# Kernel tuning notes

Measured on AMD Instinct MI355X. Metric: run time of the kernel, lower is better.

The kernel has to match this reference:

```python
import jax, jax.numpy as jnp
import numpy as np

U = 50000
I = 25000
D = 128
NUM_INTERACTIONS = 800000
NUM_LAYERS = 3


def setup_inputs() -> dict:
    key = jax.random.key(0)
    k1, k2, k3, k4 = jax.random.split(key, 4)
    # LightGCN init: nn.init.normal_(emb.weight, std=1e-4)
    user_emb = jax.random.normal(k1, (U, D), dtype=jnp.float32) * 1e-4
    item_emb = jax.random.normal(k2, (I, D), dtype=jnp.float32) * 1e-4
    # Bipartite interactions; item node ids offset by U. Symmetric adjacency.
    u = jax.random.randint(k3, (NUM_INTERACTIONS,), 0, U, dtype=jnp.int32)
    it = jax.random.randint(k4, (NUM_INTERACTIONS,), U, U + I, dtype=jnp.int32)
    edge_src = jnp.concatenate([u, it])  # [E] destination rows of adj_t
    edge_dst = jnp.concatenate([it, u])  # [E] source cols (neighbors)
    return {"user_emb": user_emb, "item_emb": item_emb,
            "edge_src": edge_src, "edge_dst": edge_dst}


def reference(user_emb, item_emb, edge_src, edge_dst):
    N = U + I
    x = jnp.concatenate([user_emb, item_emb], axis=0)  # [N, D]
    # gcn_norm without self-loops: w_ij = deg_i^-1/2 * deg_j^-1/2
    ones = jnp.ones(edge_src.shape[0], dtype=x.dtype)
    deg = jax.ops.segment_sum(ones, edge_src, num_segments=N)
    dinv = jnp.where(deg > 0, jax.lax.rsqrt(jnp.maximum(deg, 1.0)), 0.0)
    w = dinv[edge_src] * dinv[edge_dst]  # [E]
    scale = 1.0 / (NUM_LAYERS + 1)
    avg = x * scale
    for _ in range(NUM_LAYERS):
        # SpMM: out[i] = sum_{j in N(i)} w_ij * x[j]
        x = jax.ops.segment_sum(w[:, None] * x[edge_dst], edge_src, num_segments=N)
        avg = avg + x * scale
    return avg[:U], avg[U:]
```

## Files before the change

kernel.cpp:

```cpp
#include <hip/hip_runtime.h>
#include <hip/hip_fp16.h>

#define U_N 50000
#define I_N 25000
#define D_N 128
#define N_N (U_N + I_N)

#define ROWS_PER_B 256
#define NBUCK 293
#define NBLK 256
#define SN (NBUCK * NBLK)

#define SCAN_ELEMS_PER_BLOCK 1024
#define NUM_SCAN_BLOCKS ((SN + SCAN_ELEMS_PER_BLOCK - 1) / SCAN_ELEMS_PER_BLOCK)
#define SN_PAD (NUM_SCAN_BLOCKS * SCAN_ELEMS_PER_BLOCK)

typedef float f4v __attribute__((ext_vector_type(4)));
typedef float f2v __attribute__((ext_vector_type(2)));
typedef unsigned int u2v __attribute__((ext_vector_type(2)));

__global__ __launch_bounds__(256) void part_hist_kernel(const int* __restrict__ src,
                                                        int* __restrict__ hist,
                                                        int E, int chunk) {
    __shared__ int h[NBUCK];
    int t = threadIdx.x;
    for (int i = t; i < NBUCK; i += 256) h[i] = 0;
    __syncthreads();
    int b = blockIdx.x;
    int s = b * chunk;
    int e = min(E, s + chunk);
    for (int i = s + t; i < e; i += 256)
        atomicAdd(&h[src[i] >> 8], 1);
    __syncthreads();
    for (int i = t; i < NBUCK; i += 256)
        hist[i * NBLK + b] = h[i];
}

__global__ __launch_bounds__(256) void block_sums_kernel(const int4* __restrict__ cnt4,
                                                         int* __restrict__ bsums) {
    int t = threadIdx.x;
    int idx = blockIdx.x * 256 + t;
    int4 v = cnt4[idx];
    int s = v.x + v.y + v.z + v.w;
    for (int off = 32; off; off >>= 1) s += __shfl_down(s, off);
    __shared__ int wsum[4];
    int wid = t >> 6, lane = t & 63;
    if (lane == 0) wsum[wid] = s;
    __syncthreads();
    if (t == 0) bsums[blockIdx.x] = wsum[0] + wsum[1] + wsum[2] + wsum[3];
}

__global__ __launch_bounds__(128) void scan_bsums_kernel(const int* __restrict__ bsums,
                                                         int* __restrict__ boffs, int nb) {
    __shared__ int sd[128];
    int t = threadIdx.x;
    int v = (t < nb) ? bsums[t] : 0;
    sd[t] = v;
    __syncthreads();
    for (int off = 1; off < 128; off <<= 1) {
        int add = (t >= off) ? sd[t - off] : 0;
        __syncthreads();
        sd[t] += add;
        __syncthreads();
    }
    if (t < nb) boffs[t] = sd[t] - v;
}

__global__ __launch_bounds__(256) void local_scan_offs_kernel(const int4* __restrict__ cnt4,
                                                              const int* __restrict__ boffs,
                                                              int4* __restrict__ offs4) {
    int t = threadIdx.x;
    int gidx = blockIdx.x * 256 + t;
    int4 v = cnt4[gidx];
    int p0 = v.x, p1 = p0 + v.y, p2 = p1 + v.z, p3 = p2 + v.w;
    int tsum = p3;
    int lane = t & 63, wid = t >> 6;
    int incl = tsum;
    for (int off = 1; off < 64; off <<= 1) {
        int u = __shfl_up(incl, off);
        if (lane >= off) incl += u;
    }
    int lexcl = incl - tsum;
    __shared__ int wsum[4];
    if (lane == 63) wsum[wid] = incl;
    __syncthreads();
    int woff = 0;
    for (int w = 0; w < wid; ++w) woff += wsum[w];
    int base = boffs[blockIdx.x] + woff + lexcl;
    int4 o;
    o.x = base; o.y = base + p0; o.z = base + p1; o.w = base + p2;
    offs4[gidx] = o;
}

__global__ __launch_bounds__(256) void partition_kernel(const int* __restrict__ src,
                                                        const int* __restrict__ dst,
                                                        const int* __restrict__ offs,
                                                        int2* __restrict__ part,
                                                        int E, int chunk) {
    __shared__ int c[NBUCK];
    int t = threadIdx.x;
    int b = blockIdx.x;
    for (int i = t; i < NBUCK; i += 256) c[i] = offs[i * NBLK + b];
    __syncthreads();
    int s = b * chunk;
    int e = min(E, s + chunk);
    for (int i = s + t; i < e; i += 256) {
        int sv = src[i];
        int dv = dst[i];
        int pos = atomicAdd(&c[sv >> 8], 1);
        part[pos] = make_int2(sv, dv);
    }
}

__global__ __launch_bounds__(256) void bucket_csr_kernel(const int2* __restrict__ part,
                                                         const int* __restrict__ offs,
                                                         int* __restrict__ row_ptr,
                                                         float* __restrict__ dinv,
                                                         int* __restrict__ csr_dst, int E) {
    int B = blockIdx.x;
    int t = threadIdx.x;
    int bstart = offs[B * NBLK];
    int bend = (B + 1 < NBUCK) ? offs[(B + 1) * NBLK] : E;
    __shared__ int cnt_s[ROWS_PER_B];
    __shared__ int base_s[ROWS_PER_B];
    __shared__ int wsum[4];
    cnt_s[t] = 0;
    __syncthreads();
    for (int i = bstart + t; i < bend; i += 256)
        atomicAdd(&cnt_s[part[i].x & 255], 1);
    __syncthreads();
    int v = cnt_s[t];
    int lane = t & 63, wid = t >> 6;
    int incl = v;
    for (int off = 1; off < 64; off <<= 1) {
        int u = __shfl_up(incl, off);
        if (lane >= off) incl += u;
    }
    if (lane == 63) wsum[wid] = incl;
    __syncthreads();
    int woff = 0;
    for (int w = 0; w < wid; ++w) woff += wsum[w];
    int excl = woff + incl - v;
    int gid = B * ROWS_PER_B + t;
    if (gid <= N_N) row_ptr[gid] = bstart + excl;
    if (gid < N_N)  dinv[gid] = (v > 0) ? rsqrtf((float)v) : 0.0f;
    base_s[t] = bstart + excl;
    __syncthreads();
    cnt_s[t] = 0;
    __syncthreads();
    for (int i = bstart + t; i < bend; i += 256) {
        int2 ev = part[i];
        int lr = ev.x & 255;
        int pos = base_s[lr] + atomicAdd(&cnt_s[lr], 1);
        csr_dst[pos] = ev.y;
    }
}

__global__ __launch_bounds__(256) void init_kernel(const f4v* __restrict__ ue,
                                                   const f4v* __restrict__ ie,
                                                   const float* __restrict__ dinv,
                                                   __half2* __restrict__ x,
                                                   f4v* __restrict__ avg) {
    const int NU4 = U_N * D_N / 4;
    const int NT4 = N_N * D_N / 4;
    int i = blockIdx.x * blockDim.x + threadIdx.x;
    if (i >= NT4) return;
    f4v v = (i < NU4) ? ue[i] : ie[i - NU4];
    float di = dinv[i >> 5];
    f4v a = v * 0.25f;
    __builtin_nontemporal_store(a, &avg[i]);
    __half2 h0 = __floats2half2_rn(di * v.x, di * v.y);
    __half2 h1 = __floats2half2_rn(di * v.z, di * v.w);
    u2v uu = { *(unsigned int*)&h0, *(unsigned int*)&h1 };
    __builtin_nontemporal_store(uu, (u2v*)(x + 2 * (size_t)i));
}

__global__ __launch_bounds__(256) void spmm_kernel(const __half2* __restrict__ x,
                                                   __half2* __restrict__ xn,
                                                   float* __restrict__ avg,
                                                   const float* __restrict__ dinv,
                                                   const int* __restrict__ row_ptr,
                                                   const int* __restrict__ csr_dst) {
    int row = (int)((blockIdx.x * blockDim.x + threadIdx.x) >> 6);
    int lane = threadIdx.x & 63;
    int beg = __builtin_amdgcn_readfirstlane(row_ptr[row]);
    int end = __builtin_amdgcn_readfirstlane(row_ptr[row + 1]);
    float di = dinv[row];
    const __half2* xc = x + lane;
    float accx = 0.0f, accy = 0.0f;
    int k = beg;
    for (; k + 8 <= end; k += 8) {
        int j[8];
        #pragma unroll
        for (int u = 0; u < 8; ++u) j[u] = csr_dst[k + u];
        #pragma unroll
        for (int u = 0; u < 8; ++u) {
            float2 f = __half22float2(xc[(size_t)j[u] * 64]);
            accx += f.x; accy += f.y;
        }
    }
    for (; k < end; ++k) {
        float2 f = __half22float2(xc[(size_t)csr_dst[k] * 64]);
        accx += f.x; accy += f.y;
    }
    float yx = di * accx, yy = di * accy;
    float* ap = avg + (size_t)row * D_N + lane * 2;
    f2v a = __builtin_nontemporal_load((const f2v*)ap);
    a.x += 0.25f * yx;
    a.y += 0.25f * yy;
    __builtin_nontemporal_store(a, (f2v*)ap);
    __half2 h = __floats2half2_rn(di * yx, di * yy);
    __builtin_nontemporal_store(*(unsigned int*)&h,
                                (unsigned int*)(xn + (size_t)row * 64 + lane));
}

extern "C" void kernel_launch(void* const* d_in, const int* in_sizes, int n_in,
                              void* d_out, int out_size, void* d_ws, size_t ws_size,
                              hipStream_t stream) {
    const float* ue  = (const float*)d_in[0];
    const float* ie  = (const float*)d_in[1];
    const int* esrc  = (const int*)d_in[2];
    const int* edst  = (const int*)d_in[3];
    float* avg = (float*)d_out;
    const int E = in_sizes[2];
    const int N = N_N;

    char* ws = (char*)d_ws;
    size_t off = 0;
    auto alloc = [&](size_t bytes) -> void* {
        void* p = (void*)(ws + off);
        off += bytes;
        off = (off + 255) & ~((size_t)255);
        return p;
    };
    __half2* x0     = (__half2*)alloc((size_t)N * D_N * sizeof(__half));
    __half2* x1     = (__half2*)alloc((size_t)N * D_N * sizeof(__half));
    int*   hist     = (int*)  alloc((size_t)SN_PAD * sizeof(int));
    int*   offs     = (int*)  alloc((size_t)SN_PAD * sizeof(int));
    int*   row_ptr  = (int*)  alloc((size_t)(N + 1) * sizeof(int));
    float* dinv     = (float*)alloc((size_t)N * sizeof(float));
    int*   bsums    = (int*)  alloc((size_t)NUM_SCAN_BLOCKS * sizeof(int));
    int*   boffs    = (int*)  alloc((size_t)NUM_SCAN_BLOCKS * sizeof(int));
    int2*  part     = (int2*) alloc((size_t)E * sizeof(int2));
    int*   csr_dst  = (int*)  alloc((size_t)E * sizeof(int));

    hipMemsetAsync(hist, 0, (size_t)SN_PAD * sizeof(int), stream);
    int chunk = (E + NBLK - 1) / NBLK;
    part_hist_kernel<<<NBLK, 256, 0, stream>>>(esrc, hist, E, chunk);
    block_sums_kernel<<<NUM_SCAN_BLOCKS, 256, 0, stream>>>((const int4*)hist, bsums);
    scan_bsums_kernel<<<1, 128, 0, stream>>>(bsums, boffs, NUM_SCAN_BLOCKS);
    local_scan_offs_kernel<<<NUM_SCAN_BLOCKS, 256, 0, stream>>>((const int4*)hist, boffs,
                                                                (int4*)offs);
    partition_kernel<<<NBLK, 256, 0, stream>>>(esrc, edst, offs, part, E, chunk);
    bucket_csr_kernel<<<NBUCK, 256, 0, stream>>>(part, offs, row_ptr, dinv, csr_dst, E);

    const int NT4 = N * D_N / 4;
    init_kernel<<<(NT4 + 255) / 256, 256, 0, stream>>>(
        (const f4v*)ue, (const f4v*)ie, dinv, x0, (f4v*)avg);

    int sblocks = (N * 64) / 256;
    __half2* xc = x0;
    __half2* xn = x1;
    for (int layer = 0; layer < 3; ++layer) {
        spmm_kernel<<<sblocks, 256, 0, stream>>>(xc, xn, avg, dinv, row_ptr, csr_dst);
        __half2* tmp = xc; xc = xn; xn = tmp;
    }
}
```

Before: 252.9 us.

## Defer avg accumulation to final SpMM layer, removing per-layer avg read-modify-write

Intermediate SpMM layers now only write the scaled half-precision features and no longer read and write the fp32 avg buffer. The final layer reconstructs the unscaled layer outputs from the stored scaled features by dividing by dinv, reads the original embeddings, and writes avg once. This removes the fp32 avg traffic from init and the first two layers, at the cost of a third feature buffer and extra reads in the final kernel. Dividing by dinv recovers values through fp16 storage, which can amplify rounding error for rows with high degree.

```diff
diff --git a/kernel.cpp b/kernel.cpp
--- a/kernel.cpp
+++ b/kernel.cpp
@@ -159,28 +159,24 @@
 __global__ __launch_bounds__(256) void init_kernel(const f4v* __restrict__ ue,
                                                    const f4v* __restrict__ ie,
                                                    const float* __restrict__ dinv,
-                                                   __half2* __restrict__ x,
-                                                   f4v* __restrict__ avg) {
+                                                   __half2* __restrict__ x) {
     const int NU4 = U_N * D_N / 4;
     const int NT4 = N_N * D_N / 4;
     int i = blockIdx.x * blockDim.x + threadIdx.x;
     if (i >= NT4) return;
     f4v v = (i < NU4) ? ue[i] : ie[i - NU4];
     float di = dinv[i >> 5];
-    f4v a = v * 0.25f;
-    __builtin_nontemporal_store(a, &avg[i]);
     __half2 h0 = __floats2half2_rn(di * v.x, di * v.y);
     __half2 h1 = __floats2half2_rn(di * v.z, di * v.w);
     u2v uu = { *(unsigned int*)&h0, *(unsigned int*)&h1 };
-    __builtin_nontemporal_store(uu, (u2v*)(x + 2 * (size_t)i));
-}
-
-__global__ __launch_bounds__(256) void spmm_kernel(const __half2* __restrict__ x,
-                                                   __half2* __restrict__ xn,
-                                                   float* __restrict__ avg,
-                                                   const float* __restrict__ dinv,
-                                                   const int* __restrict__ row_ptr,
-                                                   const int* __restrict__ csr_dst) {
+    *(u2v*)(x + 2 * (size_t)i) = uu;
+}
+
+__global__ __launch_bounds__(256) void spmm_mid_kernel(const __half2* __restrict__ x,
+                                                       __half2* __restrict__ xn,
+                                                       const float* __restrict__ dinv,
+                                                       const int* __restrict__ row_ptr,
+                                                       const int* __restrict__ csr_dst) {
     int row = (int)((blockIdx.x * blockDim.x + threadIdx.x) >> 6);
     int lane = threadIdx.x & 63;
     int beg = __builtin_amdgcn_readfirstlane(row_ptr[row]);
@@ -203,15 +199,52 @@
         float2 f = __half22float2(xc[(size_t)csr_dst[k] * 64]);
         accx += f.x; accy += f.y;
     }
-    float yx = di * accx, yy = di * accy;
-    float* ap = avg + (size_t)row * D_N + lane * 2;
-    f2v a = __builtin_nontemporal_load((const f2v*)ap);
-    a.x += 0.25f * yx;
-    a.y += 0.25f * yy;
-    __builtin_nontemporal_store(a, (f2v*)ap);
-    __half2 h = __floats2half2_rn(di * yx, di * yy);
-    __builtin_nontemporal_store(*(unsigned int*)&h,
-                                (unsigned int*)(xn + (size_t)row * 64 + lane));
+    float s = di * di;
+    __half2 h = __floats2half2_rn(s * accx, s * accy);
+    *(unsigned int*)(xn + (size_t)row * 64 + lane) = *(unsigned int*)&h;
+}
+
+__global__ __launch_bounds__(256) void spmm_final_kernel(const __half2* __restrict__ x2p,
+                                                         const __half2* __restrict__ x1p,
+                                                         const float* __restrict__ ue,
+                                                         const float* __restrict__ ie,
+                                                         float* __restrict__ avg,
+                                                         const float* __restrict__ dinv,
+                                                         const int* __restrict__ row_ptr,
+                                                         const int* __restrict__ csr_dst) {
+    int row = (int)((blockIdx.x * blockDim.x + threadIdx.x) >> 6);
+    int lane = threadIdx.x & 63;
+    int beg = __builtin_amdgcn_readfirstlane(row_ptr[row]);
+    int end = __builtin_amdgcn_readfirstlane(row_ptr[row + 1]);
+    float di = dinv[row];
+    const __half2* xc = x2p + lane;
+    float accx = 0.0f, accy = 0.0f;
+    int k = beg;
+    for (; k + 8 <= end; k += 8) {
+        int j[8];
+        #pragma unroll
+        for (int u = 0; u < 8; ++u) j[u] = csr_dst[k + u];
+        #pragma unroll
+        for (int u = 0; u < 8; ++u) {
+            float2 f = __half22float2(xc[(size_t)j[u] * 64]);
+            accx += f.x; accy += f.y;
+        }
+    }
+    for (; k < end; ++k) {
+        float2 f = __half22float2(xc[(size_t)csr_dst[k] * 64]);
+        accx += f.x; accy += f.y;
+    }
+    float y3x = di * accx, y3y = di * accy;
+    float rs = (di > 0.0f) ? (1.0f / di) : 0.0f;
+    const float* x0r = (row < U_N) ? (ue + (size_t)row * D_N)
+                                   : (ie + (size_t)(row - U_N) * D_N);
+    f2v v0 = *(const f2v*)(x0r + lane * 2);
+    float2 f1 = __half22float2(x1p[(size_t)row * 64 + lane]);
+    float2 f2_ = __half22float2(x2p[(size_t)row * 64 + lane]);
+    f2v a;
+    a.x = 0.25f * (v0.x + rs * (f1.x + f2_.x) + y3x);
+    a.y = 0.25f * (v0.y + rs * (f1.y + f2_.y) + y3y);
+    __builtin_nontemporal_store(a, (f2v*)(avg + (size_t)row * D_N + lane * 2));
 }
 
 extern "C" void kernel_launch(void* const* d_in, const int* in_sizes, int n_in,
@@ -235,6 +268,7 @@
     };
     __half2* x0     = (__half2*)alloc((size_t)N * D_N * sizeof(__half));
     __half2* x1     = (__half2*)alloc((size_t)N * D_N * sizeof(__half));
+    __half2* x2     = (__half2*)alloc((size_t)N * D_N * sizeof(__half));
     int*   hist     = (int*)  alloc((size_t)SN_PAD * sizeof(int));
     int*   offs     = (int*)  alloc((size_t)SN_PAD * sizeof(int));
     int*   row_ptr  = (int*)  alloc((size_t)(N + 1) * sizeof(int));
@@ -256,13 +290,11 @@
 
     const int NT4 = N * D_N / 4;
     init_kernel<<<(NT4 + 255) / 256, 256, 0, stream>>>(
-        (const f4v*)ue, (const f4v*)ie, dinv, x0, (f4v*)avg);
+        (const f4v*)ue, (const f4v*)ie, dinv, x0);
 
     int sblocks = (N * 64) / 256;
-    __half2* xc = x0;
-    __half2* xn = x1;
-    for (int layer = 0; layer < 3; ++layer) {
-        spmm_kernel<<<sblocks, 256, 0, stream>>>(xc, xn, avg, dinv, row_ptr, csr_dst);
-        __half2* tmp = xc; xc = xn; xn = tmp;
-    }
-}
+    spmm_mid_kernel<<<sblocks, 256, 0, stream>>>(x0, x1, dinv, row_ptr, csr_dst);
+    spmm_mid_kernel<<<sblocks, 256, 0, stream>>>(x1, x2, dinv, row_ptr, csr_dst);
+    spmm_final_kernel<<<sblocks, 256, 0, stream>>>(x2, x1, ue, ie, avg, dinv,
+                                                   row_ptr, csr_dst);
+}
```

After: 221.0 us. 1.14x faster.
